# Optimization experiments

Hardware: AMD Instinct MI355X
Metric: run time of the kernel (lower is better)

## Reference

```python
import jax, jax.numpy as jnp
import numpy as np
import math

# Module constants derived from init_kwargs
DIM1, DIM2 = 32, 32          # n_patches = (512//16, 512//16)
PREFIX = 8                   # num_prefix_tokens
STD = 5.0                    # gauss_std
NUM_HEADS = 12               # orig_attn.num_heads (ViT-B)
EMBED_DIM = 768


def gaussian_window(n1, n2, std):
    # torch linspace(start*c, (start+(n-1))*c, n) == (arange(n)-(n-1)/2)*c
    c = 1.0 / (std * math.sqrt(2.0))
    k1 = (jnp.arange(n1, dtype=jnp.float32) - (n1 - 1) / 2.0) * c
    k2 = (jnp.arange(n2, dtype=jnp.float32) - (n2 - 1) / 2.0) * c
    return jnp.exp(-(k1[:, None] ** 2 + k2[None, :] ** 2))


def attn_addition():
    # Same-padding cross-correlation of per-token delta images with the window
    # collapses to: add[(i,l),(p,q)] = window[i-p+DIM1-1, l-q+DIM2-1]
    win = gaussian_window(2 * DIM1 - 1, 2 * DIM2 - 1, STD)
    i = jnp.arange(DIM1)
    l = jnp.arange(DIM2)
    di = i[:, None] - i[None, :] + (DIM1 - 1)   # [i, p]
    dl = l[:, None] - l[None, :] + (DIM2 - 1)   # [l, q]
    add = win[di[:, None, :, None], dl[None, :, None, :]]  # [i, l, p, q]
    add = add.reshape(DIM1 * DIM2, DIM1 * DIM2)
    # zero rows/cols for prefix tokens (prepended)
    return jnp.pad(add, ((PREFIX, 0), (PREFIX, 0)))


def setup_inputs() -> dict:
    key = jax.random.key(0)
    ks = jax.random.split(key, 5)
    B, N, C = 8, DIM1 * DIM2 + PREFIX, EMBED_DIM
    return {
        "x": jax.random.normal(ks[0], (B, N, C), dtype=jnp.float32),
        "qkv_w": jax.random.normal(ks[1], (3 * C, C), dtype=jnp.float32) * 0.02,
        "qkv_b": jax.random.normal(ks[2], (3 * C,), dtype=jnp.float32) * 0.02,
        "proj_w": jax.random.normal(ks[3], (C, C), dtype=jnp.float32) * 0.02,
        "proj_b": jax.random.normal(ks[4], (C,), dtype=jnp.float32) * 0.02,
    }


def reference(x, qkv_w, qkv_b, proj_w, proj_b):
    B, N, C = x.shape
    H = NUM_HEADS
    hd = C // H
    scale = hd ** (-0.5)
    add = attn_addition()  # [N, N] constant bias

    qkv = x @ qkv_w.T + qkv_b                      # [B, N, 3C]
    q, k, v = jnp.split(qkv, 3, axis=-1)           # q computed but unused (k.k^T attention)
    k = k.reshape(B, N, H, hd)
    v = v.reshape(B, N, H, hd)

    attn = jnp.einsum("bihd,bjhd->bhij", k, k) * scale + add[None, None]
    attn = jax.nn.softmax(attn, axis=-1)
    out = jnp.einsum("bhij,bjhd->bihd", attn, v).reshape(B, N, C)
    out = out @ proj_w.T + proj_b
    return out
```

## Files before the change

kernel.cpp:

```cpp
#include <hip/hip_runtime.h>
#include <stdint.h>

typedef __bf16 bf16;
typedef _Float16 f16;
typedef __bf16 bf16x8 __attribute__((ext_vector_type(8)));
typedef __bf16 bf16x4 __attribute__((ext_vector_type(4)));
typedef float f32x4 __attribute__((ext_vector_type(4)));

#define NSEQ 1032
#define BATCH 8
#define NHEADS 12
#define HD 64
#define CDIM 768
#define MROWS (BATCH * NSEQ)
#define PREFIX 8
#define NJT 17
#define NQ16 72
#define KSTRIDE 1152
#define VSTRIDE 1152
#define KSCALE 0.42466090f

__device__ __forceinline__ unsigned short f2bf_rne(float f) {
    union { float f; uint32_t u; } v; v.f = f;
    uint32_t u = v.u;
    return (unsigned short)((u + 0x7fffu + ((u >> 16) & 1u)) >> 16);
}

__device__ __forceinline__ void gload_lds16(const bf16* g, bf16* l) {
    __builtin_amdgcn_global_load_lds(
        (const __attribute__((address_space(1))) void*)g,
        (__attribute__((address_space(3))) void*)l, 16, 0, 0);
}

__device__ __forceinline__ void cast4(const float* src, bf16* dst, int i) {
    float4 f = ((const float4*)src)[i];
    ushort4 o;
    o.x = f2bf_rne(f.x); o.y = f2bf_rne(f.y);
    o.z = f2bf_rne(f.z); o.w = f2bf_rne(f.w);
    ((ushort4*)dst)[i] = o;
}

__device__ __forceinline__ void bar() {
    asm volatile("s_waitcnt lgkmcnt(0)" ::: "memory");
    __builtin_amdgcn_s_barrier();
    asm volatile("" ::: "memory");
}

__global__ void prep_kernel(const float* __restrict__ x,
                            const float* __restrict__ wkv,
                            const float* __restrict__ pw,
                            bf16* __restrict__ x_bf, bf16* __restrict__ wkv_bf,
                            bf16* __restrict__ pw_bf, float* __restrict__ Bias,
                            bf16* __restrict__ k_bf, bf16* __restrict__ vt_bf) {
    const int N0 = NQ16 * NJT * 1024;
    const int N1 = MROWS * CDIM / 4;
    const int N2 = 2 * CDIM * CDIM / 4;
    const int N3 = CDIM * CDIM / 4;
    const int N4 = BATCH * NHEADS * 120 * 8;
    const int N5 = BATCH * NHEADS * 64 * 15;
    int i = blockIdx.x * blockDim.x + threadIdx.x;
    if (i < N0) {
        int r    = i & 3;
        int l15  = (i >> 2) & 15;
        int quad = (i >> 6) & 3;
        int kt   = (i >> 8) & 3;
        int rest = i >> 10;
        int q16  = rest / NJT;
        int jt   = rest - q16 * NJT;
        int q = q16 * 16 + l15;
        int k = jt * 64 + kt * 16 + quad * 4 + r;
        float v;
        if (k >= NSEQ) v = -65504.f;
        else if (q < PREFIX || q >= NSEQ || k < PREFIX) v = 0.f;
        else {
            int rp = q - PREFIX, cp = k - PREFIX;
            int d1 = (rp >> 5) - (cp >> 5);
            int d2 = (rp & 31) - (cp & 31);
            v = 1.44269504f * __expf(-0.02f * (float)(d1 * d1 + d2 * d2));
        }
        Bias[i] = v;
        return;
    }
    i -= N0;
    if (i < N1) { cast4(x, x_bf, i); return; }
    i -= N1;
    if (i < N2) { cast4(wkv, wkv_bf, i); return; }
    i -= N2;
    if (i < N3) { cast4(pw, pw_bf, i); return; }
    i -= N3;
    if (i < N4) {
        int bh = i / 960, rem = i - bh * 960;
        int row = 1032 + (rem >> 3), ch = rem & 7;
        uint4 z = {0u, 0u, 0u, 0u};
        *(uint4*)&k_bf[((size_t)bh * KSTRIDE + row) * HD + ch * 8] = z;
        return;
    }
    i -= N4;
    if (i < N5) {
        int bh = i / 960, rem = i - bh * 960;
        int d = rem / 15, ch = rem - d * 15;
        uint4 z = {0u, 0u, 0u, 0u};
        *(uint4*)&vt_bf[((size_t)bh * HD + d) * VSTRIDE + 1032 + ch * 8] = z;
    }
}

template<int EPI>
__global__ __launch_bounds__(256) void gemm_nt(
    const bf16* __restrict__ A, const bf16* __restrict__ B,
    const float* __restrict__ bias,
    float* __restrict__ Cout, bf16* __restrict__ Kout, bf16* __restrict__ Vout,
    int M, int N, int K)
{
    __shared__ bf16 sA[128 * 32];
    __shared__ bf16 sB[128 * 32];
    const int t = threadIdx.x;
    const int w = t >> 6;
    const int l = t & 63;
    const int quad = l >> 4;
    const int l15 = l & 15;
    const int wy = w >> 1, wx = w & 1;
    const int m0 = blockIdx.y * 128;
    const int n0 = blockIdx.x * 128;
    const int co = (quad ^ ((l15 >> 1) & 3)) * 8;

    int r0 = t >> 2,          c0 = (t & 3) ^ ((r0 >> 1) & 3);
    int r1 = (t + 256) >> 2,  c1 = ((t + 256) & 3) ^ ((r1 >> 1) & 3);
    int ra0 = m0 + r0; if (ra0 >= M) ra0 = M - 1;
    int ra1 = m0 + r1; if (ra1 >= M) ra1 = M - 1;
    const bf16* gA0 = A + (size_t)ra0 * K + c0 * 8;
    const bf16* gA1 = A + (size_t)ra1 * K + c1 * 8;
    const bf16* gB0 = B + (size_t)(n0 + r0) * K + c0 * 8;
    const bf16* gB1 = B + (size_t)(n0 + r1) * K + c1 * 8;
    bf16* dA0 = &sA[(size_t)(w * 64) * 8];
    bf16* dA1 = &sA[(size_t)(256 + w * 64) * 8];
    bf16* dB0 = &sB[(size_t)(w * 64) * 8];
    bf16* dB1 = &sB[(size_t)(256 + w * 64) * 8];

    f32x4 acc[4][4] = {};

    for (int k0 = 0; k0 < K; k0 += 32) {
        __syncthreads();
        gload_lds16(gA0, dA0); gload_lds16(gA1, dA1);
        gload_lds16(gB0, dB0); gload_lds16(gB1, dB1);
        gA0 += 32; gA1 += 32; gB0 += 32; gB1 += 32;
        __syncthreads();
        bf16x8 af[4], bq[4];
        #pragma unroll
        for (int mt = 0; mt < 4; ++mt)
            af[mt] = *(const bf16x8*)&sA[(wy*64 + mt*16 + l15) * 32 + co];
        #pragma unroll
        for (int nt = 0; nt < 4; ++nt)
            bq[nt] = *(const bf16x8*)&sB[(wx*64 + nt*16 + l15) * 32 + co];
        #pragma unroll
        for (int mt = 0; mt < 4; ++mt)
            #pragma unroll
            for (int nt = 0; nt < 4; ++nt)
                acc[mt][nt] = __builtin_amdgcn_mfma_f32_16x16x32_bf16(af[mt], bq[nt], acc[mt][nt], 0, 0, 0);
    }

    if (EPI == 0) {
        #pragma unroll
        for (int mt = 0; mt < 4; ++mt) {
            #pragma unroll
            for (int r = 0; r < 4; ++r) {
                int m = m0 + wy*64 + mt*16 + quad*4 + r;
                if (m >= M) continue;
                #pragma unroll
                for (int nt = 0; nt < 4; ++nt) {
                    int n = n0 + wx*64 + nt*16 + l15;
                    Cout[(size_t)m * N + n] = acc[mt][nt][r] + bias[n];
                }
            }
        }
    } else {
        #pragma unroll
        for (int mt = 0; mt < 4; ++mt) {
            int mb = m0 + wy*64 + mt*16 + quad*4;
            if (mb >= M) continue;
            int b = mb / NSEQ, s = mb % NSEQ;
            #pragma unroll
            for (int nt = 0; nt < 4; ++nt) {
                int n = n0 + wx*64 + nt*16 + l15;
                float bn = bias[n];
                if (n < CDIM) {
                    int h = n >> 6, d = n & 63;
                    bf16* kp = &Kout[(((size_t)(b*NHEADS + h))*KSTRIDE + s)*HD + d];
                    #pragma unroll
                    for (int r = 0; r < 4; ++r)
                        kp[(size_t)r * HD] = (bf16)((acc[mt][nt][r] + bn) * KSCALE);
                } else {
                    int n2 = n - CDIM;
                    int h = n2 >> 6, d = n2 & 63;
                    bf16x4 pv = { (bf16)(acc[mt][nt][0] + bn), (bf16)(acc[mt][nt][1] + bn),
                                  (bf16)(acc[mt][nt][2] + bn), (bf16)(acc[mt][nt][3] + bn) };
                    *(bf16x4*)&Vout[(((size_t)(b*NHEADS + h))*HD + d)*VSTRIDE + s] = pv;
                }
            }
        }
    }
}

__global__ __launch_bounds__(256) void attn_kernel(
    const bf16* __restrict__ Kbuf, const bf16* __restrict__ VTbuf,
    const float* __restrict__ Bias, bf16* __restrict__ Hout)
{
    const int bh = blockIdx.x;
    const int b = bh / NHEADS, h = bh % NHEADS;
    const int q0 = blockIdx.y * 128;
    const bf16* Kh  = Kbuf  + (size_t)bh * KSTRIDE * HD;
    const bf16* VTh = VTbuf + (size_t)bh * HD * VSTRIDE;

    __shared__ bf16 sK[2][64 * 64];
    __shared__ bf16 sVT[2][64 * 64];
    __shared__ bf16 sP[128 * 64];

    const int t = threadIdx.x;
    const int w = t >> 6, l = t & 63, quad = l >> 4, l15 = l & 15;
    const int sw = l15 & 7;

    const int r0 = t >> 3, c0 = t & 7;
    const int r1 = r0 + 32;
    const int dk0 = r0*64 + ((c0 ^ (r0 & 7)) << 3);
    const int dk1 = r1*64 + ((c0 ^ (r1 & 7)) << 3);

    const bf16* pK0 = Kh + (size_t)r0 * HD + c0 * 8;
    const bf16* pK1 = Kh + (size_t)r1 * HD + c0 * 8;
    const bf16* pV0 = VTh + (size_t)r0 * VSTRIDE + c0 * 8;
    const bf16* pV1 = VTh + (size_t)r1 * VSTRIDE + c0 * 8;
    const float* pB0 = Bias + ((size_t)(blockIdx.y*8 + w*2 + 0) * NJT) * 1024 + quad*64 + l15*4;
    const float* pB1 = Bias + ((size_t)(blockIdx.y*8 + w*2 + 1) * NJT) * 1024 + quad*64 + l15*4;

    bf16x8 qf[2][2];
    #pragma unroll
    for (int qh = 0; qh < 2; ++qh) {
        int row = q0 + w*32 + qh*16 + l15;
        #pragma unroll
        for (int ks = 0; ks < 2; ++ks)
            qf[qh][ks] = *(const bf16x8*)&Kh[(size_t)row * HD + ks*32 + quad*8];
    }

    bf16x8 onesb;
    #pragma unroll
    for (int e = 0; e < 8; ++e) onesb[e] = (bf16)1.0f;

    f32x4 Oacc[2][4] = {};
    f32x4 Lacc[2] = {};
    const int sPr0 = (w*32 + l15) * 64;

    uint4 kva, kvb, vva, vvb;
    f32x4 bpf[2][4];

#define PREFETCH() do { \
        kva = *(const uint4*)pK0; kvb = *(const uint4*)pK1; \
        vva = *(const uint4*)pV0; vvb = *(const uint4*)pV1; \
        pK0 += 64*HD; pK1 += 64*HD; pV0 += 64; pV1 += 64; \
        _Pragma("unroll") \
        for (int kt = 0; kt < 4; ++kt) { \
            bpf[0][kt] = *(const f32x4*)(pB0 + kt*256); \
            bpf[1][kt] = *(const f32x4*)(pB1 + kt*256); \
        } \
        pB0 += 1024; pB1 += 1024; \
    } while (0)

#define ITER(CUR) do { \
        *(uint4*)&sK[CUR][dk0] = kva; *(uint4*)&sK[CUR][dk1] = kvb; \
        *(uint4*)&sVT[CUR][dk0] = vva; *(uint4*)&sVT[CUR][dk1] = vvb; \
        f32x4 sacc[2][4]; \
        _Pragma("unroll") \
        for (int qh = 0; qh < 2; ++qh) \
            _Pragma("unroll") \
            for (int kt = 0; kt < 4; ++kt) \
                sacc[qh][kt] = bpf[qh][kt]; \
        PREFETCH(); \
        bar(); \
        _Pragma("unroll") \
        for (int ks = 0; ks < 2; ++ks) { \
            bf16x8 af[4]; \
            _Pragma("unroll") \
            for (int kt = 0; kt < 4; ++kt) \
                af[kt] = *(const bf16x8*)&sK[CUR][(kt*16 + l15)*64 + (((ks*4 + quad) ^ sw) << 3)]; \
            __builtin_amdgcn_s_setprio(1); \
            _Pragma("unroll") \
            for (int qh = 0; qh < 2; ++qh) \
                _Pragma("unroll") \
                for (int kt = 0; kt < 4; ++kt) \
                    sacc[qh][kt] = __builtin_amdgcn_mfma_f32_16x16x32_bf16( \
                        af[kt], qf[qh][ks], sacc[qh][kt], 0, 0, 0); \
            __builtin_amdgcn_s_setprio(0); \
        } \
        _Pragma("unroll") \
        for (int qh = 0; qh < 2; ++qh) \
            _Pragma("unroll") \
            for (int kt = 0; kt < 4; ++kt) { \
                float p0 = __builtin_exp2f(sacc[qh][kt][0]); \
                float p1 = __builtin_exp2f(sacc[qh][kt][1]); \
                float p2 = __builtin_exp2f(sacc[qh][kt][2]); \
                float p3 = __builtin_exp2f(sacc[qh][kt][3]); \
                bf16x4 pv = { (bf16)p0, (bf16)p1, (bf16)p2, (bf16)p3 }; \
                int g = (kt*2 + (quad >> 1)) ^ sw; \
                *(bf16x4*)&sP[sPr0 + qh*1024 + g*8 + (quad & 1)*4] = pv; \
            } \
        _Pragma("unroll") \
        for (int ks = 0; ks < 2; ++ks) { \
            bf16x8 bv[4]; \
            _Pragma("unroll") \
            for (int dt = 0; dt < 4; ++dt) \
                bv[dt] = *(const bf16x8*)&sVT[CUR][(dt*16 + l15)*64 + (((ks*4 + quad) ^ sw) << 3)]; \
            __builtin_amdgcn_s_setprio(1); \
            _Pragma("unroll") \
            for (int qh = 0; qh < 2; ++qh) { \
                bf16x8 ap = *(const bf16x8*)&sP[sPr0 + qh*1024 + (((ks*4 + quad) ^ sw) * 8)]; \
                _Pragma("unroll") \
                for (int dt = 0; dt < 4; ++dt) \
                    Oacc[qh][dt] = __builtin_amdgcn_mfma_f32_16x16x32_bf16( \
                        ap, bv[dt], Oacc[qh][dt], 0, 0, 0); \
                Lacc[qh] = __builtin_amdgcn_mfma_f32_16x16x32_bf16( \
                    ap, onesb, Lacc[qh], 0, 0, 0); \
            } \
            __builtin_amdgcn_s_setprio(0); \
        } \
    } while (0)

    PREFETCH();
    ITER(0);
    #pragma unroll 1
    for (int it = 0; it < (NJT - 1) / 2; ++it) {
        ITER(1);
        ITER(0);
    }
#undef ITER
#undef PREFETCH

    #pragma unroll
    for (int qh = 0; qh < 2; ++qh)
        #pragma unroll
        for (int r = 0; r < 4; ++r) {
            int g = q0 + w*32 + qh*16 + quad*4 + r;
            if (g >= NSEQ) continue;
            float inv = 1.f / Lacc[qh][r];
            size_t base = ((size_t)(b * NSEQ) + g) * CDIM + h * HD;
            #pragma unroll
            for (int dt = 0; dt < 4; ++dt)
                Hout[base + dt*16 + l15] = (bf16)(Oacc[qh][dt][r] * inv);
        }
}

extern "C" void kernel_launch(void* const* d_in, const int* in_sizes, int n_in,
                              void* d_out, int out_size, void* d_ws, size_t ws_size,
                              hipStream_t stream) {
    const float* x      = (const float*)d_in[0];
    const float* qkv_w  = (const float*)d_in[1];
    const float* qkv_b  = (const float*)d_in[2];
    const float* proj_w = (const float*)d_in[3];
    const float* proj_b = (const float*)d_in[4];
    float* out = (float*)d_out;

    char* ws = (char*)d_ws;
    const size_t XBF_BYTES   = (size_t)MROWS * CDIM * 2;
    const size_t WKV_BYTES   = (size_t)2 * CDIM * CDIM * 2;
    const size_t PW_BYTES    = (size_t)CDIM * CDIM * 2;
    const size_t BIAS_BYTES  = (size_t)NQ16 * NJT * 1024 * 4;
    const size_t KBF_BYTES   = (size_t)BATCH * NHEADS * KSTRIDE * HD * 2;

    bf16*  x_bf   = (bf16*)ws;
    bf16*  wkv_bf = (bf16*)(ws + XBF_BYTES);
    bf16*  pw_bf  = (bf16*)(ws + XBF_BYTES + WKV_BYTES);
    float* bias_t = (float*)(ws + XBF_BYTES + WKV_BYTES + PW_BYTES);
    bf16*  k_bf   = (bf16*)(ws + XBF_BYTES + WKV_BYTES + PW_BYTES + BIAS_BYTES);
    bf16*  vt_bf  = (bf16*)(ws + XBF_BYTES + WKV_BYTES + PW_BYTES + BIAS_BYTES + KBF_BYTES);

    {
        int total = NQ16 * NJT * 1024 + MROWS * CDIM / 4
                  + 2 * CDIM * CDIM / 4 + CDIM * CDIM / 4
                  + BATCH * NHEADS * 120 * 8 + BATCH * NHEADS * 64 * 15;
        prep_kernel<<<dim3((total + 255) / 256), dim3(256), 0, stream>>>(
            x, qkv_w + (size_t)CDIM * CDIM, proj_w, x_bf, wkv_bf, pw_bf, bias_t,
            k_bf, vt_bf);
    }

    {
        dim3 grid(1536 / 128, (MROWS + 127) / 128);
        gemm_nt<1><<<grid, dim3(256), 0, stream>>>(x_bf, wkv_bf, qkv_b + CDIM,
                                                   nullptr, k_bf, vt_bf,
                                                   MROWS, 1536, CDIM);
    }

    {
        dim3 grid(BATCH * NHEADS, (NSEQ + 127) / 128);
        attn_kernel<<<grid, dim3(256), 0, stream>>>(k_bf, vt_bf, bias_t, x_bf);
    }

    {
        dim3 grid(CDIM / 128, (MROWS + 127) / 128);
        gemm_nt<0><<<grid, dim3(256), 0, stream>>>(x_bf, pw_bf, proj_b,
                                                   out, nullptr, nullptr,
                                                   MROWS, CDIM, CDIM);
    }
}
```

Before: 227.5 us.

## Double-buffer GEMM LDS tiles and ping-pong attention bias prefetch registers

The GEMM main loop now uses two LDS buffers, so the direct global-to-LDS load of the next K-slice is issued while MFMAs run on the current slice, with one vmcnt barrier per stage instead of two syncthreads. In the attention kernel, the bias prefetch goes into alternating register banks that serve directly as score accumulators, which removes the per-iteration register copy. This doubles GEMM LDS use, which may reduce occupancy, and the extra bias bank raises register pressure. The GEMM loop also assumes K is a multiple of 64.

```diff
diff --git a/kernel.cpp b/kernel.cpp
--- a/kernel.cpp
+++ b/kernel.cpp
@@ -42,6 +42,12 @@
 
 __device__ __forceinline__ void bar() {
     asm volatile("s_waitcnt lgkmcnt(0)" ::: "memory");
+    __builtin_amdgcn_s_barrier();
+    asm volatile("" ::: "memory");
+}
+
+__device__ __forceinline__ void gbar() {
+    asm volatile("s_waitcnt vmcnt(0)" ::: "memory");
     __builtin_amdgcn_s_barrier();
     asm volatile("" ::: "memory");
 }
@@ -111,8 +117,8 @@
     float* __restrict__ Cout, bf16* __restrict__ Kout, bf16* __restrict__ Vout,
     int M, int N, int K)
 {
-    __shared__ bf16 sA[128 * 32];
-    __shared__ bf16 sB[128 * 32];
+    __shared__ bf16 sA[2][128 * 32];
+    __shared__ bf16 sB[2][128 * 32];
     const int t = threadIdx.x;
     const int w = t >> 6;
     const int l = t & 63;
@@ -131,32 +137,47 @@
     const bf16* gA1 = A + (size_t)ra1 * K + c1 * 8;
     const bf16* gB0 = B + (size_t)(n0 + r0) * K + c0 * 8;
     const bf16* gB1 = B + (size_t)(n0 + r1) * K + c1 * 8;
-    bf16* dA0 = &sA[(size_t)(w * 64) * 8];
-    bf16* dA1 = &sA[(size_t)(256 + w * 64) * 8];
-    bf16* dB0 = &sB[(size_t)(w * 64) * 8];
-    bf16* dB1 = &sB[(size_t)(256 + w * 64) * 8];
+    const int oA0 = (w * 64) * 8;
+    const int oA1 = (256 + w * 64) * 8;
 
     f32x4 acc[4][4] = {};
 
-    for (int k0 = 0; k0 < K; k0 += 32) {
-        __syncthreads();
-        gload_lds16(gA0, dA0); gload_lds16(gA1, dA1);
-        gload_lds16(gB0, dB0); gload_lds16(gB1, dB1);
-        gA0 += 32; gA1 += 32; gB0 += 32; gB1 += 32;
-        __syncthreads();
-        bf16x8 af[4], bq[4];
-        #pragma unroll
-        for (int mt = 0; mt < 4; ++mt)
-            af[mt] = *(const bf16x8*)&sA[(wy*64 + mt*16 + l15) * 32 + co];
-        #pragma unroll
-        for (int nt = 0; nt < 4; ++nt)
-            bq[nt] = *(const bf16x8*)&sB[(wx*64 + nt*16 + l15) * 32 + co];
-        #pragma unroll
-        for (int mt = 0; mt < 4; ++mt)
-            #pragma unroll
-            for (int nt = 0; nt < 4; ++nt)
-                acc[mt][nt] = __builtin_amdgcn_mfma_f32_16x16x32_bf16(af[mt], bq[nt], acc[mt][nt], 0, 0, 0);
-    }
+#define STAGE(BUF) do { \
+        gload_lds16(gA0, &sA[BUF][oA0]); gload_lds16(gA1, &sA[BUF][oA1]); \
+        gload_lds16(gB0, &sB[BUF][oA0]); gload_lds16(gB1, &sB[BUF][oA1]); \
+        gA0 += 32; gA1 += 32; gB0 += 32; gB1 += 32; \
+    } while (0)
+
+#define COMPUTE(BUF) do { \
+        bf16x8 af_[4], bq_[4]; \
+        _Pragma("unroll") \
+        for (int mt = 0; mt < 4; ++mt) \
+            af_[mt] = *(const bf16x8*)&sA[BUF][(wy*64 + mt*16 + l15) * 32 + co]; \
+        _Pragma("unroll") \
+        for (int nt = 0; nt < 4; ++nt) \
+            bq_[nt] = *(const bf16x8*)&sB[BUF][(wx*64 + nt*16 + l15) * 32 + co]; \
+        _Pragma("unroll") \
+        for (int mt = 0; mt < 4; ++mt) \
+            _Pragma("unroll") \
+            for (int nt = 0; nt < 4; ++nt) \
+                acc[mt][nt] = __builtin_amdgcn_mfma_f32_16x16x32_bf16( \
+                    af_[mt], bq_[nt], acc[mt][nt], 0, 0, 0); \
+    } while (0)
+
+    STAGE(0);
+    gbar();
+    const int NP = K / 64;
+    #pragma unroll 1
+    for (int p = 0; p < NP; ++p) {
+        STAGE(1);
+        COMPUTE(0);
+        gbar();
+        if (p + 1 < NP) STAGE(0);
+        COMPUTE(1);
+        gbar();
+    }
+#undef STAGE
+#undef COMPUTE
 
     if (EPI == 0) {
         #pragma unroll
@@ -248,30 +269,28 @@
     const int sPr0 = (w*32 + l15) * 64;
 
     uint4 kva, kvb, vva, vvb;
-    f32x4 bpf[2][4];
-
-#define PREFETCH() do { \
+    f32x4 bpA[2][4], bpB[2][4];
+
+#define PREFETCH_KV() do { \
         kva = *(const uint4*)pK0; kvb = *(const uint4*)pK1; \
         vva = *(const uint4*)pV0; vvb = *(const uint4*)pV1; \
         pK0 += 64*HD; pK1 += 64*HD; pV0 += 64; pV1 += 64; \
+    } while (0)
+
+#define PREFETCH_B(BANK) do { \
         _Pragma("unroll") \
         for (int kt = 0; kt < 4; ++kt) { \
-            bpf[0][kt] = *(const f32x4*)(pB0 + kt*256); \
-            bpf[1][kt] = *(const f32x4*)(pB1 + kt*256); \
+            BANK[0][kt] = *(const f32x4*)(pB0 + kt*256); \
+            BANK[1][kt] = *(const f32x4*)(pB1 + kt*256); \
         } \
         pB0 += 1024; pB1 += 1024; \
     } while (0)
 
-#define ITER(CUR) do { \
+#define ITER(CUR, ACC, NEXT) do { \
         *(uint4*)&sK[CUR][dk0] = kva; *(uint4*)&sK[CUR][dk1] = kvb; \
         *(uint4*)&sVT[CUR][dk0] = vva; *(uint4*)&sVT[CUR][dk1] = vvb; \
-        f32x4 sacc[2][4]; \
-        _Pragma("unroll") \
-        for (int qh = 0; qh < 2; ++qh) \
-            _Pragma("unroll") \
-            for (int kt = 0; kt < 4; ++kt) \
-                sacc[qh][kt] = bpf[qh][kt]; \
-        PREFETCH(); \
+        PREFETCH_KV(); \
+        PREFETCH_B(NEXT); \
         bar(); \
         _Pragma("unroll") \
         for (int ks = 0; ks < 2; ++ks) { \
@@ -284,18 +303,18 @@
             for (int qh = 0; qh < 2; ++qh) \
                 _Pragma("unroll") \
                 for (int kt = 0; kt < 4; ++kt) \
-                    sacc[qh][kt] = __builtin_amdgcn_mfma_f32_16x16x32_bf16( \
-                        af[kt], qf[qh][ks], sacc[qh][kt], 0, 0, 0); \
+                    ACC[qh][kt] = __builtin_amdgcn_mfma_f32_16x16x32_bf16( \
+                        af[kt], qf[qh][ks], ACC[qh][kt], 0, 0, 0); \
             __builtin_amdgcn_s_setprio(0); \
         } \
         _Pragma("unroll") \
         for (int qh = 0; qh < 2; ++qh) \
             _Pragma("unroll") \
             for (int kt = 0; kt < 4; ++kt) { \
-                float p0 = __builtin_exp2f(sacc[qh][kt][0]); \
-                float p1 = __builtin_exp2f(sacc[qh][kt][1]); \
-                float p2 = __builtin_exp2f(sacc[qh][kt][2]); \
-                float p3 = __builtin_exp2f(sacc[qh][kt][3]); \
+                float p0 = __builtin_exp2f(ACC[qh][kt][0]); \
+                float p1 = __builtin_exp2f(ACC[qh][kt][1]); \
+                float p2 = __builtin_exp2f(ACC[qh][kt][2]); \
+                float p3 = __builtin_exp2f(ACC[qh][kt][3]); \
                 bf16x4 pv = { (bf16)p0, (bf16)p1, (bf16)p2, (bf16)p3 }; \
                 int g = (kt*2 + (quad >> 1)) ^ sw; \
                 *(bf16x4*)&sP[sPr0 + qh*1024 + g*8 + (quad & 1)*4] = pv; \
@@ -321,15 +340,17 @@
         } \
     } while (0)
 
-    PREFETCH();
-    ITER(0);
+    PREFETCH_KV();
+    PREFETCH_B(bpA);
+    ITER(0, bpA, bpB);
     #pragma unroll 1
     for (int it = 0; it < (NJT - 1) / 2; ++it) {
-        ITER(1);
-        ITER(0);
+        ITER(1, bpB, bpA);
+        ITER(0, bpA, bpB);
     }
 #undef ITER
-#undef PREFETCH
+#undef PREFETCH_KV
+#undef PREFETCH_B
 
     #pragma unroll
     for (int qh = 0; qh < 2; ++qh)
```

After: 225.6 us. Within noise of the previous version (-0.8%).
